# Kernel tuning notes

Measured on AMD Instinct MI355X. Metric: run time of the kernel, lower is better.

Reference implementation:

```python
import jax, jax.numpy as jnp
import numpy as np


def _shift_gather(x, s, axis):
    """Gather x shifted by integer offset s along `axis`, zero outside bounds.

    Matches deform_conv2d's zero-padding bilinear-corner semantics: each
    integer corner outside [0, n) contributes zero.
    """
    n = x.shape[axis]
    idx = jnp.arange(n) + s                      # traced integer shift
    valid = (idx >= 0) & (idx < n)
    g = jnp.take(x, jnp.clip(idx, 0, n - 1), axis=axis)
    bshape = [1] * x.ndim
    bshape[axis] = n
    return g * valid.reshape(bshape).astype(x.dtype)


def _axial_deform_dw(x, taps_w, r_val, axis):
    """Depthwise 1D conv along `axis` with fractional (learned) dilation.

    For tap k_pos in [-P, P], deform_conv2d samples at base + k_pos + k_pos*(r-1)
    = base + k_pos * r, i.e. a constant fractional shift per tap, realized via
    bilinear interpolation between the two neighboring integer rows/cols.
    taps_w: (C, K) depthwise weights along the given spatial axis.
    """
    K = taps_w.shape[1]
    P = K // 2
    out = jnp.zeros_like(x)
    for i in range(K):
        k_pos = i - P
        delta = k_pos * r_val                    # fractional sampling shift (traced)
        d0f = jnp.floor(delta)
        frac = (delta - d0f).astype(x.dtype)
        d0 = d0f.astype(jnp.int32)
        s0 = _shift_gather(x, d0, axis)
        s1 = _shift_gather(x, d0 + 1, axis)
        samp = (1.0 - frac) * s0 + frac * s1     # bilinear along the axis
        out = out + samp * taps_w[:, i][None, :, None, None]
    return out


def reference(x, weight_h, weight_w, r):
    # r is clamped to >= 1 as in the torch module
    r_val = jnp.clip(r, 1.0)
    wh = weight_h[:, 0, :, 0]                    # (C, kh) vertical taps
    ww = weight_w[:, 0, 0, :]                    # (C, kw) horizontal taps
    out_h = _axial_deform_dw(x, wh, r_val, axis=2)  # deform conv along H
    out_w = _axial_deform_dw(x, ww, r_val, axis=3)  # deform conv along W
    return x + out_h + out_w


def setup_inputs() -> dict:
    key = jax.random.key(0)
    k0, k1, k2 = jax.random.split(key, 3)
    B, C, H, W, KH, KW = 8, 128, 224, 224, 7, 7
    x = jax.random.normal(k0, (B, C, H, W), dtype=jnp.float32)
    # kaiming_normal fan_out scale ~ sqrt(2 / (C * K))
    weight_h = jax.random.normal(k1, (C, 1, KH, 1), dtype=jnp.float32) * np.sqrt(2.0 / (C * KH))
    weight_w = jax.random.normal(k2, (C, 1, 1, KW), dtype=jnp.float32) * np.sqrt(2.0 / (C * KW))
    r = jnp.asarray(1.7, dtype=jnp.float32)      # learned dilation parameter
    return {"x": x, "weight_h": weight_h, "weight_w": weight_w, "r": r}
```

## Files before the change

kernel.cpp:

```cpp
#include <hip/hip_runtime.h>
#include <stdint.h>


namespace {
constexpr int B = 8, C = 128, H = 224, W = 224;
constexpr int KT = 7;
constexpr int M  = 6;
constexpr int NT = 2 * M + 1;
constexpr int TH = 16;
constexpr int NTPB = 7;
constexpr int SROWS = TH + 2 * M;
constexpr int WQ = W / 4;
constexpr int BLOCK = 448;
constexpr int RPT = 2;
constexpr int WROWS = RPT + 2 * M;
constexpr int RSTRIDE = 228;
constexpr int BUF_FLOATS = SROWS * RSTRIDE;
constexpr int LDS_FLOATS = 2 * BUF_FLOATS;
constexpr int ZOFF = 2 * C * NT;
}

typedef __attribute__((address_space(3))) uint32_t lds_u32;
typedef __attribute__((address_space(1))) const uint32_t gbl_u32;

__global__ void taps_kernel(const float* __restrict__ wh, const float* __restrict__ ww,
                            const float* __restrict__ r, float* __restrict__ taps) {
    int c = threadIdx.x;
    if (c >= C) return;
    taps[ZOFF + c]     = 0.f;
    taps[ZOFF + C + c] = 0.f;
    float rv = fmaxf(r[0], 1.0f);
    float eh[NT], ew[NT];
    for (int j = 0; j < NT; ++j) { eh[j] = 0.f; ew[j] = 0.f; }
    for (int i = 0; i < KT; ++i) {
        float kpos  = (float)(i - KT / 2);
        float delta = kpos * rv;
        float d0f   = floorf(delta);
        float fr    = delta - d0f;
        int   j0    = (int)d0f + M;
        float whv = wh[c * KT + i];
        float wwv = ww[c * KT + i];
        if (j0 >= 0 && j0 < NT)         { eh[j0]   += (1.f - fr) * whv; ew[j0]   += (1.f - fr) * wwv; }
        if (j0 + 1 >= 0 && j0 + 1 < NT) { eh[j0+1] += fr * whv;         ew[j0+1] += fr * wwv; }
    }
    for (int j = 0; j < NT; ++j) {
        taps[c * NT + j]          = eh[j];
        taps[C * NT + c * NT + j] = ew[j];
    }
}

__global__ __launch_bounds__(BLOCK) void deform_axial_kernel(
    const float* __restrict__ x, const float* __restrict__ taps,
    float* __restrict__ out) {
    __shared__ float lds[LDS_FLOATS];

    const int bid   = blockIdx.x;
    const int p     = bid >> 1;
    const int half  = bid & 1;
    const int hbase = half * (H / 2);
    const int c     = p & (C - 1);
    const int tid   = threadIdx.x;
    const int wave  = tid >> 6;
    const int lane  = tid & 63;

    const long base = (long)p * (H * W);
    const float* __restrict__ xp = x + base;

    float eh[NT], ew[NT];
    const float* __restrict__ ehp = taps + c * NT;
    const float* __restrict__ ewp = taps + C * NT + c * NT;
#pragma unroll
    for (int j = 0; j < NT; ++j) { eh[j] = ehp[j]; ew[j] = ewp[j]; }
    const float ws6 = ew[6] + 1.0f;
    asm volatile("s_waitcnt vmcnt(0)" ::: "memory");

    const float* zbase = taps + ZOFF + lane * 4;
    float* const buf0 = lds;
    float* const buf1 = lds + BUF_FLOATS;

    auto STAGE = [&](float* bufb, int t) {
        const int h0 = hbase + t * TH;
#pragma unroll
        for (int k = 0; k < 4; ++k) {
            const int row  = k * 7 + wave;
            const int grow = h0 - M + row;
            const bool vr  = (unsigned)grow < (unsigned)H;
            const float* src = vr ? (xp + grow * W + lane * 4) : zbase;
            float* dst = bufb + row * RSTRIDE;
            if (lane < 56) {
                __builtin_amdgcn_global_load_lds((gbl_u32*)src, (lds_u32*)dst, 16, 0, 0);
            }
        }
    };

    auto BAR = []() {
        asm volatile("" ::: "memory");
        __builtin_amdgcn_s_barrier();
        asm volatile("" ::: "memory");
    };

    const int cq = tid % WQ;
    const int rg = tid / WQ;
    const int r0 = rg * RPT;
    const float4 zero4 = make_float4(0.f, 0.f, 0.f, 0.f);

    auto COMPUTE = [&](const float* ldsb, int t) {
        const int h0 = hbase + t * TH;
        float4 acc[RPT];
#pragma unroll
        for (int k = 0; k < RPT; ++k) acc[k] = zero4;

#pragma unroll
        for (int s = 0; s < WROWS; ++s) {
            const float4 q = *reinterpret_cast<const float4*>(&ldsb[(r0 + s) * RSTRIDE + cq * 4]);

#pragma unroll
            for (int k = 0; k < RPT; ++k) {
                const int j = s - k;
                if (j >= 0 && j < NT) {
                    const float wgt = eh[j];
                    acc[k].x = fmaf(wgt, q.x, acc[k].x);
                    acc[k].y = fmaf(wgt, q.y, acc[k].y);
                    acc[k].z = fmaf(wgt, q.z, acc[k].z);
                    acc[k].w = fmaf(wgt, q.w, acc[k].w);
                }
            }

            if (s >= M && s < M + RPT) {
                const int k = s - M;
                const float* crow = &ldsb[(r0 + s) * RSTRIDE];
                float4& a = acc[k];

                {
                    const float4 qd = (cq >= 2) ? *reinterpret_cast<const float4*>(crow + (cq - 2) * 4) : zero4;
                    a.x = fmaf(ew[0], qd.z, a.x);
                    a.x = fmaf(ew[1], qd.w, a.x);
                    a.y = fmaf(ew[0], qd.w, a.y);
                }
                {
                    const float4 qd = (cq >= 1) ? *reinterpret_cast<const float4*>(crow + (cq - 1) * 4) : zero4;
                    a.x = fmaf(ew[2], qd.x, a.x); a.y = fmaf(ew[1], qd.x, a.y); a.z = fmaf(ew[0], qd.x, a.z);
                    a.x = fmaf(ew[3], qd.y, a.x); a.y = fmaf(ew[2], qd.y, a.y); a.z = fmaf(ew[1], qd.y, a.z); a.w = fmaf(ew[0], qd.y, a.w);
                    a.x = fmaf(ew[4], qd.z, a.x); a.y = fmaf(ew[3], qd.z, a.y); a.z = fmaf(ew[2], qd.z, a.z); a.w = fmaf(ew[1], qd.z, a.w);
                    a.x = fmaf(ew[5], qd.w, a.x); a.y = fmaf(ew[4], qd.w, a.y); a.z = fmaf(ew[3], qd.w, a.z); a.w = fmaf(ew[2], qd.w, a.w);
                }
                {
                    a.x = fmaf(ws6,   q.x, a.x); a.y = fmaf(ew[5], q.x, a.y); a.z = fmaf(ew[4], q.x, a.z); a.w = fmaf(ew[3], q.x, a.w);
                    a.x = fmaf(ew[7], q.y, a.x); a.y = fmaf(ws6,   q.y, a.y); a.z = fmaf(ew[5], q.y, a.z); a.w = fmaf(ew[4], q.y, a.w);
                    a.x = fmaf(ew[8], q.z, a.x); a.y = fmaf(ew[7], q.z, a.y); a.z = fmaf(ws6,   q.z, a.z); a.w = fmaf(ew[5], q.z, a.w);
                    a.x = fmaf(ew[9], q.w, a.x); a.y = fmaf(ew[8], q.w, a.y); a.z = fmaf(ew[7], q.w, a.z); a.w = fmaf(ws6,   q.w, a.w);
                }
                {
                    const float4 qd = (cq <= WQ - 2) ? *reinterpret_cast<const float4*>(crow + (cq + 1) * 4) : zero4;
                    a.x = fmaf(ew[10], qd.x, a.x); a.y = fmaf(ew[9],  qd.x, a.y); a.z = fmaf(ew[8],  qd.x, a.z); a.w = fmaf(ew[7],  qd.x, a.w);
                    a.x = fmaf(ew[11], qd.y, a.x); a.y = fmaf(ew[10], qd.y, a.y); a.z = fmaf(ew[9],  qd.y, a.z); a.w = fmaf(ew[8],  qd.y, a.w);
                    a.x = fmaf(ew[12], qd.z, a.x); a.y = fmaf(ew[11], qd.z, a.y); a.z = fmaf(ew[10], qd.z, a.z); a.w = fmaf(ew[9],  qd.z, a.w);
                                                   a.y = fmaf(ew[12], qd.w, a.y); a.z = fmaf(ew[11], qd.w, a.z); a.w = fmaf(ew[10], qd.w, a.w);
                }
                {
                    const float4 qd = (cq <= WQ - 3) ? *reinterpret_cast<const float4*>(crow + (cq + 2) * 4) : zero4;
                    a.z = fmaf(ew[12], qd.x, a.z);
                    a.w = fmaf(ew[11], qd.x, a.w);
                    a.w = fmaf(ew[12], qd.y, a.w);
                }
            }
        }

        float* outp = out + base + (long)(h0 + r0) * W + cq * 4;
#pragma unroll
        for (int k = 0; k < RPT; ++k) {
            *reinterpret_cast<float4*>(outp + k * W) = acc[k];
        }
    };

    STAGE(buf0, 0);
    STAGE(buf1, 1);
    asm volatile("s_waitcnt vmcnt(4)" ::: "memory");
    BAR();
    COMPUTE(buf0, 0);
    BAR();

#pragma unroll
    for (int t = 1; t <= NTPB - 2; ++t) {
        STAGE((t & 1) ? buf0 : buf1, t + 1);
        asm volatile("s_waitcnt vmcnt(6)" ::: "memory");
        BAR();
        COMPUTE((t & 1) ? buf1 : buf0, t);
        BAR();
    }

    asm volatile("s_waitcnt vmcnt(2)" ::: "memory");
    BAR();
    COMPUTE(buf0, NTPB - 1);
}

extern "C" void kernel_launch(void* const* d_in, const int* in_sizes, int n_in,
                              void* d_out, int out_size, void* d_ws, size_t ws_size,
                              hipStream_t stream) {
    const float* x  = (const float*)d_in[0];
    const float* wh = (const float*)d_in[1];
    const float* ww = (const float*)d_in[2];
    const float* r  = (const float*)d_in[3];
    float* out  = (float*)d_out;
    float* taps = (float*)d_ws;

    hipLaunchKernelGGL(taps_kernel, dim3(1), dim3(C), 0, stream, wh, ww, r, taps);
    hipLaunchKernelGGL(deform_axial_kernel, dim3(2 * B * C), dim3(BLOCK),
                       0, stream, x, taps, out);
}
```

Before: 98.55 us.

## Map waves to row groups and exchange horizontal neighbors via cross-lane shuffles

The block grows from 448 to 512 threads so each wave owns one pair of output rows, with its lane index as the column quad. The horizontal-tap neighbor float4 reads from LDS are replaced by __shfl exchanges of the centre value, with edge lanes zeroed. Staging now spreads rows over 8 waves, and the spare slots reload duplicate rows. Lanes 56-63 sit idle during compute, and the shuffles lower to ds_bpermute, which still goes through LDS hardware and adds more instructions than the vector reads it replaces.

After: 103.1 us. 4.6% more time.

```diff
diff --git a/kernel.cpp b/kernel.cpp
--- a/kernel.cpp
+++ b/kernel.cpp
@@ -11,7 +11,7 @@
 constexpr int NTPB = 7;
 constexpr int SROWS = TH + 2 * M;
 constexpr int WQ = W / 4;
-constexpr int BLOCK = 448;
+constexpr int BLOCK = 512;
 constexpr int RPT = 2;
 constexpr int WROWS = RPT + 2 * M;
 constexpr int RSTRIDE = 228;
@@ -82,7 +82,8 @@
         const int h0 = hbase + t * TH;
 #pragma unroll
         for (int k = 0; k < 4; ++k) {
-            const int row  = k * 7 + wave;
+            int row = k * 8 + wave;
+            if (row >= SROWS) row = wave;
             const int grow = h0 - M + row;
             const bool vr  = (unsigned)grow < (unsigned)H;
             const float* src = vr ? (xp + grow * W + lane * 4) : zbase;
@@ -99,9 +100,8 @@
         asm volatile("" ::: "memory");
     };
 
-    const int cq = tid % WQ;
-    const int rg = tid / WQ;
-    const int r0 = rg * RPT;
+    const int cq = lane;
+    const int r0 = wave * RPT;
     const float4 zero4 = make_float4(0.f, 0.f, 0.f, 0.f);
 
     auto COMPUTE = [&](const float* ldsb, int t) {
@@ -128,21 +128,32 @@
 
             if (s >= M && s < M + RPT) {
                 const int k = s - M;
-                const float* crow = &ldsb[(r0 + s) * RSTRIDE];
                 float4& a = acc[k];
 
-                {
-                    const float4 qd = (cq >= 2) ? *reinterpret_cast<const float4*>(crow + (cq - 2) * 4) : zero4;
-                    a.x = fmaf(ew[0], qd.z, a.x);
-                    a.x = fmaf(ew[1], qd.w, a.x);
-                    a.y = fmaf(ew[0], qd.w, a.y);
-                }
-                {
-                    const float4 qd = (cq >= 1) ? *reinterpret_cast<const float4*>(crow + (cq - 1) * 4) : zero4;
-                    a.x = fmaf(ew[2], qd.x, a.x); a.y = fmaf(ew[1], qd.x, a.y); a.z = fmaf(ew[0], qd.x, a.z);
-                    a.x = fmaf(ew[3], qd.y, a.x); a.y = fmaf(ew[2], qd.y, a.y); a.z = fmaf(ew[1], qd.y, a.z); a.w = fmaf(ew[0], qd.y, a.w);
-                    a.x = fmaf(ew[4], qd.z, a.x); a.y = fmaf(ew[3], qd.z, a.y); a.z = fmaf(ew[2], qd.z, a.z); a.w = fmaf(ew[1], qd.z, a.w);
-                    a.x = fmaf(ew[5], qd.w, a.x); a.y = fmaf(ew[4], qd.w, a.y); a.z = fmaf(ew[3], qd.w, a.z); a.w = fmaf(ew[2], qd.w, a.w);
+                float4 qm1, qp1;
+                qm1.x = __shfl(q.x, lane - 1); qm1.y = __shfl(q.y, lane - 1);
+                qm1.z = __shfl(q.z, lane - 1); qm1.w = __shfl(q.w, lane - 1);
+                qp1.x = __shfl(q.x, lane + 1); qp1.y = __shfl(q.y, lane + 1);
+                qp1.z = __shfl(q.z, lane + 1); qp1.w = __shfl(q.w, lane + 1);
+                float qm2z = __shfl(q.z, lane - 2);
+                float qm2w = __shfl(q.w, lane - 2);
+                float qp2x = __shfl(q.x, lane + 2);
+                float qp2y = __shfl(q.y, lane + 2);
+                if (cq < 1)      qm1 = zero4;
+                if (cq < 2)      { qm2z = 0.f; qm2w = 0.f; }
+                if (cq > WQ - 2) qp1 = zero4;
+                if (cq > WQ - 3) { qp2x = 0.f; qp2y = 0.f; }
+
+                {
+                    a.x = fmaf(ew[0], qm2z, a.x);
+                    a.x = fmaf(ew[1], qm2w, a.x);
+                    a.y = fmaf(ew[0], qm2w, a.y);
+                }
+                {
+                    a.x = fmaf(ew[2], qm1.x, a.x); a.y = fmaf(ew[1], qm1.x, a.y); a.z = fmaf(ew[0], qm1.x, a.z);
+                    a.x = fmaf(ew[3], qm1.y, a.x); a.y = fmaf(ew[2], qm1.y, a.y); a.z = fmaf(ew[1], qm1.y, a.z); a.w = fmaf(ew[0], qm1.y, a.w);
+                    a.x = fmaf(ew[4], qm1.z, a.x); a.y = fmaf(ew[3], qm1.z, a.y); a.z = fmaf(ew[2], qm1.z, a.z); a.w = fmaf(ew[1], qm1.z, a.w);
+                    a.x = fmaf(ew[5], qm1.w, a.x); a.y = fmaf(ew[4], qm1.w, a.y); a.z = fmaf(ew[3], qm1.w, a.z); a.w = fmaf(ew[2], qm1.w, a.w);
                 }
                 {
                     a.x = fmaf(ws6,   q.x, a.x); a.y = fmaf(ew[5], q.x, a.y); a.z = fmaf(ew[4], q.x, a.z); a.w = fmaf(ew[3], q.x, a.w);
@@ -151,17 +162,15 @@
                     a.x = fmaf(ew[9], q.w, a.x); a.y = fmaf(ew[8], q.w, a.y); a.z = fmaf(ew[7], q.w, a.z); a.w = fmaf(ws6,   q.w, a.w);
                 }
                 {
-                    const float4 qd = (cq <= WQ - 2) ? *reinterpret_cast<const float4*>(crow + (cq + 1) * 4) : zero4;
-                    a.x = fmaf(ew[10], qd.x, a.x); a.y = fmaf(ew[9],  qd.x, a.y); a.z = fmaf(ew[8],  qd.x, a.z); a.w = fmaf(ew[7],  qd.x, a.w);
-                    a.x = fmaf(ew[11], qd.y, a.x); a.y = fmaf(ew[10], qd.y, a.y); a.z = fmaf(ew[9],  qd.y, a.z); a.w = fmaf(ew[8],  qd.y, a.w);
-                    a.x = fmaf(ew[12], qd.z, a.x); a.y = fmaf(ew[11], qd.z, a.y); a.z = fmaf(ew[10], qd.z, a.z); a.w = fmaf(ew[9],  qd.z, a.w);
-                                                   a.y = fmaf(ew[12], qd.w, a.y); a.z = fmaf(ew[11], qd.w, a.z); a.w = fmaf(ew[10], qd.w, a.w);
-                }
-                {
-                    const float4 qd = (cq <= WQ - 3) ? *reinterpret_cast<const float4*>(crow + (cq + 2) * 4) : zero4;
-                    a.z = fmaf(ew[12], qd.x, a.z);
-                    a.w = fmaf(ew[11], qd.x, a.w);
-                    a.w = fmaf(ew[12], qd.y, a.w);
+                    a.x = fmaf(ew[10], qp1.x, a.x); a.y = fmaf(ew[9],  qp1.x, a.y); a.z = fmaf(ew[8],  qp1.x, a.z); a.w = fmaf(ew[7],  qp1.x, a.w);
+                    a.x = fmaf(ew[11], qp1.y, a.x); a.y = fmaf(ew[10], qp1.y, a.y); a.z = fmaf(ew[9],  qp1.y, a.z); a.w = fmaf(ew[8],  qp1.y, a.w);
+                    a.x = fmaf(ew[12], qp1.z, a.x); a.y = fmaf(ew[11], qp1.z, a.y); a.z = fmaf(ew[10], qp1.z, a.z); a.w = fmaf(ew[9],  qp1.z, a.w);
+                                                    a.y = fmaf(ew[12], qp1.w, a.y); a.z = fmaf(ew[11], qp1.w, a.z); a.w = fmaf(ew[10], qp1.w, a.w);
+                }
+                {
+                    a.z = fmaf(ew[12], qp2x, a.z);
+                    a.w = fmaf(ew[11], qp2x, a.w);
+                    a.w = fmaf(ew[12], qp2y, a.w);
                 }
             }
         }
@@ -177,7 +186,7 @@
     STAGE(buf1, 1);
     asm volatile("s_waitcnt vmcnt(4)" ::: "memory");
     BAR();
-    COMPUTE(buf0, 0);
+    if (lane < 56) COMPUTE(buf0, 0);
     BAR();
 
 #pragma unroll
@@ -185,13 +194,13 @@
         STAGE((t & 1) ? buf0 : buf1, t + 1);
         asm volatile("s_waitcnt vmcnt(6)" ::: "memory");
         BAR();
-        COMPUTE((t & 1) ? buf1 : buf0, t);
+        if (lane < 56) COMPUTE((t & 1) ? buf1 : buf0, t);
         BAR();
     }
 
     asm volatile("s_waitcnt vmcnt(2)" ::: "memory");
     BAR();
-    COMPUTE(buf0, NTPB - 1);
+    if (lane < 56) COMPUTE(buf0, NTPB - 1);
 }
 
 extern "C" void kernel_launch(void* const* d_in, const int* in_sizes, int n_in,
```
